# Kernel optimization log

Measured on AMD Instinct MI355X. Metric: run time of the kernel, lower is better.

## Reference

```python
import jax, jax.numpy as jnp
import numpy as np

HIDDEN = 6      # tiny MLP width
GRID_R = 16     # CAM grid resolution
NUM_LAYERS = 2  # num hidden layers == shared_cam.num_layers
OUT_DIM = 3
N_POINTS = 2_097_152
LN_EPS = 1e-5


def _bilinear_border(grid, xy):
    """F.grid_sample(mode='bilinear', padding_mode='border', align_corners=True)
    for point queries. grid: [C, R, R]; xy: [N, 2] in [-1, 1] with xy[:,0]=x
    (width) and xy[:,1]=y (height). Returns [N, C]."""
    R = grid.shape[-1]
    # align_corners=True mapping to pixel coords, border padding = clamp
    coords = jnp.clip((xy + 1.0) * 0.5 * (R - 1), 0.0, float(R - 1))
    ix, iy = coords[:, 0], coords[:, 1]
    x0f, y0f = jnp.floor(ix), jnp.floor(iy)
    wx, wy = ix - x0f, iy - y0f                       # [N]
    x0 = x0f.astype(jnp.int32)
    y0 = y0f.astype(jnp.int32)
    x1 = jnp.minimum(x0 + 1, R - 1)
    y1 = jnp.minimum(y0 + 1, R - 1)
    g00 = grid[:, y0, x0]  # [C, N]
    g01 = grid[:, y0, x1]
    g10 = grid[:, y1, x0]
    g11 = grid[:, y1, x1]
    top = g00 * (1.0 - wx) + g01 * wx
    bot = g10 * (1.0 - wx) + g11 * wx
    return (top * (1.0 - wy) + bot * wy).T            # [N, C]


def _layernorm(h, w, b):
    mu = jnp.mean(h, axis=-1, keepdims=True)
    var = jnp.mean((h - mu) ** 2, axis=-1, keepdims=True)  # biased, like torch LN
    return (h - mu) * jax.lax.rsqrt(var + LN_EPS) * w + b


def setup_inputs() -> dict:
    key = jax.random.key(0)
    ks = jax.random.split(key, 10)
    xy = jax.random.uniform(ks[0], (N_POINTS, 2), dtype=jnp.float32,
                            minval=-1.0, maxval=1.0)
    # CAM grids (init is ones/zeros; perturb so the math is exercised)
    gamma = 1.0 + 0.1 * jax.random.normal(ks[1], (NUM_LAYERS, HIDDEN, GRID_R, GRID_R), jnp.float32)
    beta = 0.1 * jax.random.normal(ks[2], (NUM_LAYERS, HIDDEN, GRID_R, GRID_R), jnp.float32)
    # Tiny MLP weights (Kaiming-ish scale)
    w_in = jax.random.normal(ks[3], (HIDDEN, 2), jnp.float32) / np.sqrt(2.0)
    b_in = 0.1 * jax.random.normal(ks[4], (HIDDEN,), jnp.float32)
    w_h = jax.random.normal(ks[5], (NUM_LAYERS - 1, HIDDEN, HIDDEN), jnp.float32) / np.sqrt(HIDDEN)
    b_h = 0.1 * jax.random.normal(ks[6], (NUM_LAYERS - 1, HIDDEN), jnp.float32)
    w_out = jax.random.normal(ks[7], (OUT_DIM, HIDDEN), jnp.float32) / np.sqrt(HIDDEN)
    b_out = 0.1 * jax.random.normal(ks[8], (OUT_DIM,), jnp.float32)
    ln_w = 1.0 + 0.05 * jax.random.normal(ks[9], (NUM_LAYERS, HIDDEN), jnp.float32)
    ln_b = jnp.zeros((NUM_LAYERS, HIDDEN), jnp.float32)
    return {"xy": xy, "gamma": gamma, "beta": beta, "w_in": w_in, "b_in": b_in,
            "w_h": w_h, "b_h": b_h, "w_out": w_out, "b_out": b_out,
            "ln_w": ln_w, "ln_b": ln_b}


def reference(xy, gamma, beta, w_in, b_in, w_h, b_h, w_out, b_out, ln_w, ln_b):
    # h = act(in_layer(xy))
    h = jax.nn.silu(xy @ w_in.T + b_in)                    # [N, HIDDEN]
    for i in range(NUM_LAYERS):
        if i > 0:
            h = jax.nn.silu(h @ w_h[i - 1].T + b_h[i - 1])
        g = _bilinear_border(gamma[i], xy)                 # [N, HIDDEN]
        bb = _bilinear_border(beta[i], xy)                 # [N, HIDDEN]
        h = g * _layernorm(h, ln_w[i], ln_b[i]) + bb
    return h @ w_out.T + b_out                             # [N, OUT_DIM]
```

## Files before the change

kernel.cpp:

```cpp
#include <hip/hip_runtime.h>
#include <hip/hip_fp16.h>
#include <stdint.h>

#define NPTS 2097152
#define BLOCK 256
#define PPT 4
#define NBLK (NPTS / (BLOCK * PPT))

static __device__ __forceinline__ float silu_f(float v) {
    return v * __builtin_amdgcn_rcpf(1.0f + __expf(-v));
}
static __device__ __forceinline__ __half2 u2h(uint32_t u) {
    union { uint32_t i; __half2 h; } v; v.i = u; return v.h;
}
static __device__ __forceinline__ uint32_t h2u(__half2 h) {
    union { __half2 h; uint32_t i; } v; v.h = h; return v.i;
}

__global__ __launch_bounds__(BLOCK, 4) void camfield_kernel(
    const float* __restrict__ xy,
    const float* __restrict__ gamma,
    const float* __restrict__ beta,
    const float* __restrict__ w_in,
    const float* __restrict__ b_in,
    const float* __restrict__ w_h,
    const float* __restrict__ b_h,
    const float* __restrict__ w_out,
    const float* __restrict__ b_out,
    const float* __restrict__ ln_w,
    const float* __restrict__ ln_b,
    float* __restrict__ out)
{
    __shared__ __align__(16) uint32_t sg[2][256][12];

    const int tid = threadIdx.x;

    for (int idx = tid; idx < 3072; idx += BLOCK) {
        int l = (idx >= 1536) ? 1 : 0;
        int r = idx - l * 1536;
        int s = r >> 8;
        int cell = r & 255;
        int x = cell & 15;
        int x1 = (x < 15) ? x + 1 : 15;
        int rowb = cell - x;
        const float* src = (s < 3) ? (gamma + l * 1536 + (2 * s) * 256)
                                   : (beta  + l * 1536 + (2 * (s - 3)) * 256);
        float a_lo = src[rowb + x];
        float a_hi = src[256 + rowb + x];
        float b_lo = src[rowb + x1];
        float b_hi = src[256 + rowb + x1];
        sg[l][cell][2 * s]     = h2u(__floats2half2_rn(a_lo, a_hi));
        sg[l][cell][2 * s + 1] = h2u(__floats2half2_rn(b_lo, b_hi));
    }

    float Win0[6], Win1[6], Bin[6], Wh[6][6], Bh[6], Wo[3][6], Bo[3], LnW[2][6], LnB[2][6];
#pragma unroll
    for (int j = 0; j < 6; ++j) {
        Win0[j] = w_in[2 * j];
        Win1[j] = w_in[2 * j + 1];
        Bin[j]  = b_in[j];
        Bh[j]   = b_h[j];
#pragma unroll
        for (int k = 0; k < 6; ++k) Wh[j][k] = w_h[6 * j + k];
        LnW[0][j] = ln_w[j];     LnW[1][j] = ln_w[6 + j];
        LnB[0][j] = ln_b[j];     LnB[1][j] = ln_b[6 + j];
    }
#pragma unroll
    for (int j = 0; j < 3; ++j) {
        Bo[j] = b_out[j];
#pragma unroll
        for (int k = 0; k < 6; ++k) Wo[j][k] = w_out[6 * j + k];
    }

    __syncthreads();

    const int p0 = (blockIdx.x * BLOCK + tid) * PPT;

    const float4* xv = (const float4*)(xy + 2 * p0);
    float4 q0 = xv[0];
    float4 q1 = xv[1];
    float xs[4] = { q0.x, q0.z, q1.x, q1.z };
    float ys[4] = { q0.y, q0.w, q1.y, q1.w };

    float o[3 * PPT];

#pragma unroll
    for (int p = 0; p < PPT; ++p) {
        const float x = xs[p];
        const float y = ys[p];

        float fx = fminf(fmaxf(fmaf(x, 7.5f, 7.5f), 0.0f), 15.0f);
        float fy = fminf(fmaxf(fmaf(y, 7.5f, 7.5f), 0.0f), 15.0f);
        int x0 = (int)fx; if (x0 > 14) x0 = 14;
        int y0 = (int)fy; if (y0 > 14) y0 = 14;
        float wx = fx - (float)x0;
        float wy = fy - (float)y0;
        float w11f = wx * wy;
        float w10f = wy - w11f;
        float w01f = wx - w11f;
        float w00f = 1.0f - wx - wy + w11f;

        const __half2 W00 = __float2half2_rn(w00f);
        const __half2 W01 = __float2half2_rn(w01f);
        const __half2 W10 = __float2half2_rn(w10f);
        const __half2 W11 = __float2half2_rn(w11f);

        const int cell = (y0 << 4) + x0;

        float gl[2][6], bl[2][6];
#pragma unroll
        for (int l = 0; l < 2; ++l) {
            const uint4* c4 = (const uint4*)&sg[l][cell][0];
            uint4 u0 = c4[0];
            uint4 u1 = c4[1];
            uint4 u2 = c4[2];
            uint4 v0 = c4[48];
            uint4 v1 = c4[49];
            uint4 v2 = c4[50];

            uint32_t A[6] = { u0.x, u0.z, u1.x, u1.z, u2.x, u2.z };
            uint32_t B[6] = { u0.y, u0.w, u1.y, u1.w, u2.y, u2.w };
            uint32_t C[6] = { v0.x, v0.z, v1.x, v1.z, v2.x, v2.z };
            uint32_t D[6] = { v0.y, v0.w, v1.y, v1.w, v2.y, v2.w };

            float2 r[6];
#pragma unroll
            for (int s = 0; s < 6; ++s) {
                __half2 acc = __hmul2(u2h(A[s]), W00);
                acc = __hfma2(u2h(B[s]), W01, acc);
                acc = __hfma2(u2h(C[s]), W10, acc);
                acc = __hfma2(u2h(D[s]), W11, acc);
                r[s] = __half22float2(acc);
            }
            gl[l][0] = r[0].x; gl[l][1] = r[0].y;
            gl[l][2] = r[1].x; gl[l][3] = r[1].y;
            gl[l][4] = r[2].x; gl[l][5] = r[2].y;
            bl[l][0] = r[3].x; bl[l][1] = r[3].y;
            bl[l][2] = r[4].x; bl[l][3] = r[4].y;
            bl[l][4] = r[5].x; bl[l][5] = r[5].y;
        }

        float h[6];
#pragma unroll
        for (int j = 0; j < 6; ++j)
            h[j] = silu_f(fmaf(x, Win0[j], fmaf(y, Win1[j], Bin[j])));

        {
            float mu = (h[0] + h[1] + h[2] + h[3] + h[4] + h[5]) * (1.0f / 6.0f);
            float d[6], var = 0.0f;
#pragma unroll
            for (int j = 0; j < 6; ++j) { d[j] = h[j] - mu; var = fmaf(d[j], d[j], var); }
            var *= (1.0f / 6.0f);
            float rs = __builtin_amdgcn_rsqf(var + 1e-5f);
#pragma unroll
            for (int j = 0; j < 6; ++j)
                h[j] = fmaf(gl[0][j], fmaf(d[j] * rs, LnW[0][j], LnB[0][j]), bl[0][j]);
        }

        float t[6];
#pragma unroll
        for (int j = 0; j < 6; ++j) {
            float a = Bh[j];
#pragma unroll
            for (int k = 0; k < 6; ++k) a = fmaf(h[k], Wh[j][k], a);
            t[j] = silu_f(a);
        }

        {
            float mu = (t[0] + t[1] + t[2] + t[3] + t[4] + t[5]) * (1.0f / 6.0f);
            float d[6], var = 0.0f;
#pragma unroll
            for (int j = 0; j < 6; ++j) { d[j] = t[j] - mu; var = fmaf(d[j], d[j], var); }
            var *= (1.0f / 6.0f);
            float rs = __builtin_amdgcn_rsqf(var + 1e-5f);
#pragma unroll
            for (int j = 0; j < 6; ++j)
                t[j] = fmaf(gl[1][j], fmaf(d[j] * rs, LnW[1][j], LnB[1][j]), bl[1][j]);
        }

#pragma unroll
        for (int j = 0; j < 3; ++j) {
            float a = Bo[j];
#pragma unroll
            for (int k = 0; k < 6; ++k) a = fmaf(t[k], Wo[j][k], a);
            o[3 * p + j] = a;
        }
    }

    float4* op = (float4*)(out + 3 * p0);
#pragma unroll
    for (int q = 0; q < 3; ++q)
        op[q] = make_float4(o[4 * q], o[4 * q + 1], o[4 * q + 2], o[4 * q + 3]);
}

extern "C" void kernel_launch(void* const* d_in, const int* in_sizes, int n_in,
                              void* d_out, int out_size, void* d_ws, size_t ws_size,
                              hipStream_t stream) {
    camfield_kernel<<<NBLK, BLOCK, 0, stream>>>(
        (const float*)d_in[0],
        (const float*)d_in[1],
        (const float*)d_in[2],
        (const float*)d_in[3],
        (const float*)d_in[4],
        (const float*)d_in[5],
        (const float*)d_in[6],
        (const float*)d_in[7],
        (const float*)d_in[8],
        (const float*)d_in[9],
        (const float*)d_in[10],
        (float*)d_out);
}
```

Baseline: 109.9 us.

## Fold LayerNorm affine into CAM grids and stage per-layer grid loads

Pre-multiplies gamma by ln_w and folds ln_b into beta while building the fp16 shared-memory table. The per-point LayerNorm then needs only one fma per channel instead of two. It also forces the MLP weights to be wave-uniform via readfirstlane, so they can sit in scalar registers and ease VGPR pressure. Finally it defers the layer-1 grid loads until after layer 0, which shortens live ranges. Rounding the folded products to fp16 slightly changes numerics.

```diff
diff --git a/kernel.cpp b/kernel.cpp
--- a/kernel.cpp
+++ b/kernel.cpp
@@ -10,11 +10,48 @@
 static __device__ __forceinline__ float silu_f(float v) {
     return v * __builtin_amdgcn_rcpf(1.0f + __expf(-v));
 }
+static __device__ __forceinline__ float rfl(float v) {
+    return __int_as_float(__builtin_amdgcn_readfirstlane(__float_as_int(v)));
+}
 static __device__ __forceinline__ __half2 u2h(uint32_t u) {
     union { uint32_t i; __half2 h; } v; v.i = u; return v.h;
 }
 static __device__ __forceinline__ uint32_t h2u(__half2 h) {
     union { __half2 h; uint32_t i; } v; v.h = h; return v.i;
+}
+
+static __device__ __forceinline__ void interp6(
+    uint4 u0, uint4 u1, uint4 u2, uint4 v0, uint4 v1, uint4 v2,
+    __half2 W00, __half2 W01, __half2 W10, __half2 W11,
+    float* g, float* b)
+{
+    uint32_t A[6] = { u0.x, u0.z, u1.x, u1.z, u2.x, u2.z };
+    uint32_t Bv[6] = { u0.y, u0.w, u1.y, u1.w, u2.y, u2.w };
+    uint32_t C[6] = { v0.x, v0.z, v1.x, v1.z, v2.x, v2.z };
+    uint32_t D[6] = { v0.y, v0.w, v1.y, v1.w, v2.y, v2.w };
+#pragma unroll
+    for (int s = 0; s < 6; ++s) {
+        __half2 acc = __hmul2(u2h(A[s]), W00);
+        acc = __hfma2(u2h(Bv[s]), W01, acc);
+        acc = __hfma2(u2h(C[s]), W10, acc);
+        acc = __hfma2(u2h(D[s]), W11, acc);
+        float2 r = __half22float2(acc);
+        if (s < 3) { g[2 * s] = r.x; g[2 * s + 1] = r.y; }
+        else       { b[2 * (s - 3)] = r.x; b[2 * (s - 3) + 1] = r.y; }
+    }
+}
+
+static __device__ __forceinline__ void ln_apply(float* h, const float* g, const float* b)
+{
+    float mu = (h[0] + h[1] + h[2] + h[3] + h[4] + h[5]) * (1.0f / 6.0f);
+    float d[6], var = 0.0f;
+#pragma unroll
+    for (int j = 0; j < 6; ++j) { d[j] = h[j] - mu; var = fmaf(d[j], d[j], var); }
+    var *= (1.0f / 6.0f);
+    float rs = __builtin_amdgcn_rsqf(var + 1e-5f);
+#pragma unroll
+    for (int j = 0; j < 6; ++j)
+        h[j] = fmaf(g[j], d[j] * rs, b[j]);
 }
 
 __global__ __launch_bounds__(BLOCK, 4) void camfield_kernel(
@@ -43,33 +80,46 @@
         int x = cell & 15;
         int x1 = (x < 15) ? x + 1 : 15;
         int rowb = cell - x;
-        const float* src = (s < 3) ? (gamma + l * 1536 + (2 * s) * 256)
-                                   : (beta  + l * 1536 + (2 * (s - 3)) * 256);
-        float a_lo = src[rowb + x];
-        float a_hi = src[256 + rowb + x];
-        float b_lo = src[rowb + x1];
-        float b_hi = src[256 + rowb + x1];
+        int ch0 = (s < 3) ? 2 * s : 2 * (s - 3);
+        const float* gsrc = gamma + l * 1536 + ch0 * 256;
+        float ga_lo = gsrc[rowb + x];
+        float ga_hi = gsrc[256 + rowb + x];
+        float gb_lo = gsrc[rowb + x1];
+        float gb_hi = gsrc[256 + rowb + x1];
+        float a_lo, a_hi, b_lo, b_hi;
+        if (s < 3) {
+            float w_lo = ln_w[6 * l + ch0];
+            float w_hi = ln_w[6 * l + ch0 + 1];
+            a_lo = ga_lo * w_lo; a_hi = ga_hi * w_hi;
+            b_lo = gb_lo * w_lo; b_hi = gb_hi * w_hi;
+        } else {
+            const float* bsrc = beta + l * 1536 + ch0 * 256;
+            float nb_lo = ln_b[6 * l + ch0];
+            float nb_hi = ln_b[6 * l + ch0 + 1];
+            a_lo = fmaf(ga_lo, nb_lo, bsrc[rowb + x]);
+            a_hi = fmaf(ga_hi, nb_hi, bsrc[256 + rowb + x]);
+            b_lo = fmaf(gb_lo, nb_lo, bsrc[rowb + x1]);
+            b_hi = fmaf(gb_hi, nb_hi, bsrc[256 + rowb + x1]);
+        }
         sg[l][cell][2 * s]     = h2u(__floats2half2_rn(a_lo, a_hi));
         sg[l][cell][2 * s + 1] = h2u(__floats2half2_rn(b_lo, b_hi));
     }
 
-    float Win0[6], Win1[6], Bin[6], Wh[6][6], Bh[6], Wo[3][6], Bo[3], LnW[2][6], LnB[2][6];
+    float Win0[6], Win1[6], Bin[6], Wh[6][6], Bh[6], Wo[3][6], Bo[3];
 #pragma unroll
     for (int j = 0; j < 6; ++j) {
         Win0[j] = w_in[2 * j];
         Win1[j] = w_in[2 * j + 1];
         Bin[j]  = b_in[j];
-        Bh[j]   = b_h[j];
-#pragma unroll
-        for (int k = 0; k < 6; ++k) Wh[j][k] = w_h[6 * j + k];
-        LnW[0][j] = ln_w[j];     LnW[1][j] = ln_w[6 + j];
-        LnB[0][j] = ln_b[j];     LnB[1][j] = ln_b[6 + j];
+        Bh[j]   = rfl(b_h[j]);
+#pragma unroll
+        for (int k = 0; k < 6; ++k) Wh[j][k] = rfl(w_h[6 * j + k]);
     }
 #pragma unroll
     for (int j = 0; j < 3; ++j) {
-        Bo[j] = b_out[j];
-#pragma unroll
-        for (int k = 0; k < 6; ++k) Wo[j][k] = w_out[6 * j + k];
+        Bo[j] = rfl(b_out[j]);
+#pragma unroll
+        for (int k = 0; k < 6; ++k) Wo[j][k] = rfl(w_out[6 * j + k]);
     }
 
     __syncthreads();
@@ -106,56 +156,30 @@
         const __half2 W11 = __float2half2_rn(w11f);
 
         const int cell = (y0 << 4) + x0;
-
-        float gl[2][6], bl[2][6];
-#pragma unroll
-        for (int l = 0; l < 2; ++l) {
-            const uint4* c4 = (const uint4*)&sg[l][cell][0];
-            uint4 u0 = c4[0];
-            uint4 u1 = c4[1];
-            uint4 u2 = c4[2];
-            uint4 v0 = c4[48];
-            uint4 v1 = c4[49];
-            uint4 v2 = c4[50];
-
-            uint32_t A[6] = { u0.x, u0.z, u1.x, u1.z, u2.x, u2.z };
-            uint32_t B[6] = { u0.y, u0.w, u1.y, u1.w, u2.y, u2.w };
-            uint32_t C[6] = { v0.x, v0.z, v1.x, v1.z, v2.x, v2.z };
-            uint32_t D[6] = { v0.y, v0.w, v1.y, v1.w, v2.y, v2.w };
-
-            float2 r[6];
-#pragma unroll
-            for (int s = 0; s < 6; ++s) {
-                __half2 acc = __hmul2(u2h(A[s]), W00);
-                acc = __hfma2(u2h(B[s]), W01, acc);
-                acc = __hfma2(u2h(C[s]), W10, acc);
-                acc = __hfma2(u2h(D[s]), W11, acc);
-                r[s] = __half22float2(acc);
-            }
-            gl[l][0] = r[0].x; gl[l][1] = r[0].y;
-            gl[l][2] = r[1].x; gl[l][3] = r[1].y;
-            gl[l][4] = r[2].x; gl[l][5] = r[2].y;
-            bl[l][0] = r[3].x; bl[l][1] = r[3].y;
-            bl[l][2] = r[4].x; bl[l][3] = r[4].y;
-            bl[l][4] = r[5].x; bl[l][5] = r[5].y;
-        }
+        const uint4* c4 = (const uint4*)&sg[0][cell][0];
+
+        uint4 u0 = c4[0];
+        uint4 u1 = c4[1];
+        uint4 u2 = c4[2];
+        uint4 v0 = c4[48];
+        uint4 v1 = c4[49];
+        uint4 v2 = c4[50];
 
         float h[6];
 #pragma unroll
         for (int j = 0; j < 6; ++j)
             h[j] = silu_f(fmaf(x, Win0[j], fmaf(y, Win1[j], Bin[j])));
 
-        {
-            float mu = (h[0] + h[1] + h[2] + h[3] + h[4] + h[5]) * (1.0f / 6.0f);
-            float d[6], var = 0.0f;
-#pragma unroll
-            for (int j = 0; j < 6; ++j) { d[j] = h[j] - mu; var = fmaf(d[j], d[j], var); }
-            var *= (1.0f / 6.0f);
-            float rs = __builtin_amdgcn_rsqf(var + 1e-5f);
-#pragma unroll
-            for (int j = 0; j < 6; ++j)
-                h[j] = fmaf(gl[0][j], fmaf(d[j] * rs, LnW[0][j], LnB[0][j]), bl[0][j]);
-        }
+        float g0[6], b0[6];
+        interp6(u0, u1, u2, v0, v1, v2, W00, W01, W10, W11, g0, b0);
+        ln_apply(h, g0, b0);
+
+        uint4 a0 = c4[768];
+        uint4 a1 = c4[769];
+        uint4 a2 = c4[770];
+        uint4 c0 = c4[816];
+        uint4 c1 = c4[817];
+        uint4 c2 = c4[818];
 
         float t[6];
 #pragma unroll
@@ -166,17 +190,9 @@
             t[j] = silu_f(a);
         }
 
-        {
-            float mu = (t[0] + t[1] + t[2] + t[3] + t[4] + t[5]) * (1.0f / 6.0f);
-            float d[6], var = 0.0f;
-#pragma unroll
-            for (int j = 0; j < 6; ++j) { d[j] = t[j] - mu; var = fmaf(d[j], d[j], var); }
-            var *= (1.0f / 6.0f);
-            float rs = __builtin_amdgcn_rsqf(var + 1e-5f);
-#pragma unroll
-            for (int j = 0; j < 6; ++j)
-                t[j] = fmaf(gl[1][j], fmaf(d[j] * rs, LnW[1][j], LnB[1][j]), bl[1][j]);
-        }
+        float g1[6], b1[6];
+        interp6(a0, a1, a2, c0, c1, c2, W00, W01, W10, W11, g1, b1);
+        ln_apply(t, g1, b1);
 
 #pragma unroll
         for (int j = 0; j < 3; ++j) {
```

Result: no change. 110.1 us (+0.2%).
